# Kernel optimization log

Hardware: AMD Instinct MI355X
Metric: run time of the kernel (lower is better)

Reference implementation:

```python
import jax, jax.numpy as jnp
import numpy as np

# Module constants from __init__: z_max=32, ppm=2 -> delta=0.5, z_min=delta=0.5, log_prob=True
Z_MIN = 0.5
Z_MAX = 32.0
DELTA = 0.5


def _depth_positions(S):
    # depth_steps = arange(z_min, z_max + delta, delta) -> Z=64 bins in [0.5, 32]
    depth_steps = jnp.arange(Z_MIN, Z_MAX + DELTA, DELTA)
    log_steps = jnp.log2(depth_steps)
    log_min = np.log2(Z_MIN)
    log_max = np.log2(Z_MAX)
    norm = (log_steps - log_min) / (log_max - log_min)  # in [0, 1]
    # grid_sample align_corners=True maps [-1,1] -> [0, S-1]; norm*2-1 -> norm*(S-1)
    return norm * (S - 1)  # (Z,)


def setup_inputs() -> dict:
    key = jax.random.key(0)
    k1, k2 = jax.random.split(key)
    image = jax.random.normal(k1, (32, 64, 64, 128), dtype=jnp.float32)          # (B,D,H,W)
    polar_log_depths = jax.random.normal(k2, (32, 64, 128, 64), dtype=jnp.float32)  # (B,H,W,S)
    return {"image": image, "polar_log_depths": polar_log_depths}


def reference(image, polar_log_depths):
    S = polar_log_depths.shape[-1]
    pos = _depth_positions(S)                                 # (Z,) fixed interp positions
    i0 = jnp.clip(jnp.floor(pos).astype(jnp.int32), 0, S - 1)
    i1 = jnp.clip(i0 + 1, 0, S - 1)
    w = pos - i0.astype(pos.dtype)                            # linear weights; w=0 at right edge
    v0 = jnp.take(polar_log_depths, i0, axis=-1)              # (B,H,W,Z)
    v1 = jnp.take(polar_log_depths, i1, axis=-1)
    depth_scores = v0 * (1.0 - w) + v1 * w                    # 1D linear interp == grid_sample here

    # log_prob=True branch: softmax / logsumexp over height axis (dim=1)
    depth_prob = jax.nn.softmax(depth_scores, axis=1)         # (B,H,W,Z)
    cell_score = jax.nn.logsumexp(depth_scores, axis=1)       # (B,W,Z)

    # einsum '...dhw,...hwz->...dzw': weighted reduction over height
    image_polar = jnp.einsum('bdhw,bhwz->bdzw', image, depth_prob)  # (B,D,Z,W)
    return image_polar, cell_score
```

## Files before the change

### kernel.cpp

```cpp
#include <hip/hip_runtime.h>
#include <hip/hip_bf16.h>
#include <math.h>

#define B_ 32
#define D_ 64
#define H_ 64
#define W_ 128
#define S_ 64
#define Z_ 64
#define WT 4

typedef __attribute__((ext_vector_type(8))) short bf16x8;
typedef __attribute__((ext_vector_type(4))) float f32x4;

static __device__ __forceinline__ short f2bf(float f) {
    union { __hip_bfloat16 h; short s; } u;
    u.h = __float2bfloat16(f);
    return u.s;
}
static __device__ __forceinline__ float getc(const float4& v, int k) {
    switch (k) { case 0: return v.x; case 1: return v.y; case 2: return v.z; default: return v.w; }
}

static __device__ __forceinline__ int swz(int w, int row, int oct) {
    return w * 8192 + row * 128 + (((oct ^ row ^ w) & 7) << 4);
}

__global__ __launch_bounds__(1024, 8)
void polar_proj_kernel(const float* __restrict__ image,
                       const float* __restrict__ polar,
                       float* __restrict__ out_img,
                       float* __restrict__ out_cell) {
    __shared__ __align__(16) unsigned char sP[WT * 8192];
    __shared__ __align__(16) unsigned char sA[WT * 8192];

    const int t = threadIdx.x;

    const int cpx = gridDim.x >> 3;
    const int logical = (blockIdx.x & 7) * cpx + (blockIdx.x >> 3);
    const int b  = logical >> 5;
    const int w0 = (logical & 31) << 2;

    const int d_im = t >> 4;
    const int h0   = (t & 15) << 2;
    float4 ir[4];
#pragma unroll
    for (int k = 0; k < 4; ++k)
        ir[k] = *(const float4*)(image + ((size_t)((b * D_ + d_im) * H_ + h0 + k)) * W_ + w0);

    const int q4  = t & 3;
    const int rr  = t >> 2;
    const int w_p = rr >> 6, h_p = rr & 63;
    const float* src = polar + ((size_t)((b * H_ + h_p) * W_ + w0 + w_p)) * S_ + q4 * 16;
    float4 pr[4];
#pragma unroll
    for (int k = 0; k < 4; ++k)
        pr[k] = *(const float4*)(src + k * 4);

#pragma unroll
    for (int w = 0; w < 4; ++w) {
        const short s0 = f2bf(getc(ir[0], w));
        const short s1 = f2bf(getc(ir[1], w));
        const short s2 = f2bf(getc(ir[2], w));
        const short s3 = f2bf(getc(ir[3], w));
        int2 pk;
        pk.x = (s0 & 0xffff) | (s1 << 16);
        pk.y = (s2 & 0xffff) | (s3 << 16);
        *(int2*)(sA + swz(w, d_im, h0 >> 3) + ((h0 & 7) << 1)) = pk;
    }

#pragma unroll
    for (int c = 0; c < 2; ++c) {
        bf16x8 v;
#pragma unroll
        for (int e = 0; e < 8; ++e)
            v[e] = f2bf(getc(pr[c * 2 + (e >> 2)], e & 3));
        *(bf16x8*)(sP + swz(w_p, h_p, q4 * 2 + c)) = v;
    }
    __syncthreads();

    const int lane = t & 63;
    const int wv   = t >> 6;
    const int fr   = lane & 15, lg = lane >> 4;
    const int wS   = wv >> 2, zq = wv & 3;

    const int z = zq * 16 + fr;
    const float posf = (log2f(0.5f + 0.5f * (float)z) + 1.0f) * 10.5f;
    int i0 = (int)floorf(posf);
    i0 = i0 < 0 ? 0 : (i0 > S_ - 1 ? S_ - 1 : i0);
    const int i1 = (i0 + 1 > S_ - 1) ? (S_ - 1) : (i0 + 1);
    const float wz = posf - (float)i0;

    bf16x8 bw[2];
#pragma unroll
    for (int ks = 0; ks < 2; ++ks)
#pragma unroll
        for (int e = 0; e < 8; ++e) {
            const int s = ks * 32 + lg * 8 + e;
            const float v = (s == i0 ? 1.0f - wz : 0.0f) + (s == i1 ? wz : 0.0f);
            bw[ks][e] = f2bf(v);
        }

    f32x4 sacc[4] = {};
#pragma unroll
    for (int ks = 0; ks < 2; ++ks)
#pragma unroll
        for (int mt = 0; mt < 4; ++mt) {
            const bf16x8 a = *(const bf16x8*)(sP + swz(wS, mt * 16 + fr, ks * 4 + lg));
            sacc[mt] = __builtin_amdgcn_mfma_f32_16x16x32_bf16(a, bw[ks], sacc[mt], 0, 0, 0);
        }

    float ex[4][4];
    float ss = 0.0f;
#pragma unroll
    for (int mt = 0; mt < 4; ++mt)
#pragma unroll
        for (int r = 0; r < 4; ++r) {
            const float e = __expf(sacc[mt][r]);
            ex[mt][r] = e;
            ss += e;
        }
    ss += __shfl_xor(ss, 16);
    ss += __shfl_xor(ss, 32);
    if (lg == 0)
        out_cell[((size_t)b * W_ + w0 + wS) * Z_ + z] = __logf(ss);
    const float inv = 1.0f / ss;
    __syncthreads();

#pragma unroll
    for (int mt = 0; mt < 4; ++mt) {
        const short p0 = f2bf(ex[mt][0] * inv);
        const short p1 = f2bf(ex[mt][1] * inv);
        const short p2 = f2bf(ex[mt][2] * inv);
        const short p3 = f2bf(ex[mt][3] * inv);
        int2 pk;
        pk.x = (p0 & 0xffff) | (p1 << 16);
        pk.y = (p2 & 0xffff) | (p3 << 16);
        *(int2*)(sP + swz(wS, z, mt * 2 + (lg >> 1)) + ((lg & 1) << 3)) = pk;
    }
    __syncthreads();

    const int mtp = wv >> 2, ntp = wv & 3;
    f32x4 acc[4] = {};
#pragma unroll
    for (int w = 0; w < 4; ++w)
#pragma unroll
        for (int ks = 0; ks < 2; ++ks) {
            const bf16x8 a  = *(const bf16x8*)(sA + swz(w, mtp * 16 + fr, ks * 4 + lg));
            const bf16x8 bb = *(const bf16x8*)(sP + swz(w, ntp * 16 + fr, ks * 4 + lg));
            acc[w] = __builtin_amdgcn_mfma_f32_16x16x32_bf16(a, bb, acc[w], 0, 0, 0);
        }

#pragma unroll
    for (int r = 0; r < 4; ++r) {
        const int d  = mtp * 16 + lg * 4 + r;
        const int zc = ntp * 16 + fr;
        float4 o;
        o.x = acc[0][r];
        o.y = acc[1][r];
        o.z = acc[2][r];
        o.w = acc[3][r];
        *(float4*)(out_img + ((size_t)((b * D_ + d) * Z_) + zc) * W_ + w0) = o;
    }
}

extern "C" void kernel_launch(void* const* d_in, const int* in_sizes, int n_in,
                              void* d_out, int out_size, void* d_ws, size_t ws_size,
                              hipStream_t stream) {
    const float* image = (const float*)d_in[0];
    const float* polar = (const float*)d_in[1];
    float* out_img  = (float*)d_out;
    float* out_cell = out_img + (size_t)B_ * D_ * Z_ * W_;
    dim3 grid(B_ * (W_ / WT));
    polar_proj_kernel<<<grid, 1024, 0, stream>>>(image, polar, out_img, out_cell);
}
```

Measured before the change: 51.12 us.

## Split into softmax-prob kernel and wide-W PV matmul kernel with stashed probabilities

The single fused kernel becomes two. The first computes the interpolated scores, the softmax and the logsumexp, then writes bf16 probabilities into the output buffer as a scratch stash. The second loads a 16-wide W slab of the image, reads the stashed probabilities, runs the MFMA reduction over height, and transposes the results through LDS so each output row is written as a wider contiguous segment. The aim is to replace the scattered 16-byte output stores with wider coalesced ones, at the cost of an extra global write and read of the probabilities, a second launch, and lower occupancy from the larger LDS footprint.

After: 56.78 us. +11.1%, slower.

```diff
diff --git a/kernel.cpp b/kernel.cpp
--- a/kernel.cpp
+++ b/kernel.cpp
@@ -8,7 +8,6 @@
 #define W_ 128
 #define S_ 64
 #define Z_ 64
-#define WT 4
 
 typedef __attribute__((ext_vector_type(8))) short bf16x8;
 typedef __attribute__((ext_vector_type(4))) float f32x4;
@@ -27,48 +26,26 @@
 }
 
 __global__ __launch_bounds__(1024, 8)
-void polar_proj_kernel(const float* __restrict__ image,
-                       const float* __restrict__ polar,
+void polar_prob_kernel(const float* __restrict__ polar,
                        float* __restrict__ out_img,
                        float* __restrict__ out_cell) {
-    __shared__ __align__(16) unsigned char sP[WT * 8192];
-    __shared__ __align__(16) unsigned char sA[WT * 8192];
+    __shared__ __align__(16) unsigned char sP[4 * 8192];
 
     const int t = threadIdx.x;
-
     const int cpx = gridDim.x >> 3;
     const int logical = (blockIdx.x & 7) * cpx + (blockIdx.x >> 3);
-    const int b  = logical >> 5;
-    const int w0 = (logical & 31) << 2;
-
-    const int d_im = t >> 4;
-    const int h0   = (t & 15) << 2;
-    float4 ir[4];
-#pragma unroll
-    for (int k = 0; k < 4; ++k)
-        ir[k] = *(const float4*)(image + ((size_t)((b * D_ + d_im) * H_ + h0 + k)) * W_ + w0);
-
-    const int q4  = t & 3;
-    const int rr  = t >> 2;
+    const int b   = logical >> 5;
+    const int wt4 = logical & 31;
+    const int w0  = wt4 << 2;
+
+    const int q4 = t & 3;
+    const int rr = t >> 2;
     const int w_p = rr >> 6, h_p = rr & 63;
     const float* src = polar + ((size_t)((b * H_ + h_p) * W_ + w0 + w_p)) * S_ + q4 * 16;
     float4 pr[4];
 #pragma unroll
     for (int k = 0; k < 4; ++k)
         pr[k] = *(const float4*)(src + k * 4);
-
-#pragma unroll
-    for (int w = 0; w < 4; ++w) {
-        const short s0 = f2bf(getc(ir[0], w));
-        const short s1 = f2bf(getc(ir[1], w));
-        const short s2 = f2bf(getc(ir[2], w));
-        const short s3 = f2bf(getc(ir[3], w));
-        int2 pk;
-        pk.x = (s0 & 0xffff) | (s1 << 16);
-        pk.y = (s2 & 0xffff) | (s3 << 16);
-        *(int2*)(sA + swz(w, d_im, h0 >> 3) + ((h0 & 7) << 1)) = pk;
-    }
-
 #pragma unroll
     for (int c = 0; c < 2; ++c) {
         bf16x8 v;
@@ -83,8 +60,7 @@
     const int wv   = t >> 6;
     const int fr   = lane & 15, lg = lane >> 4;
     const int wS   = wv >> 2, zq = wv & 3;
-
-    const int z = zq * 16 + fr;
+    const int z    = zq * 16 + fr;
     const float posf = (log2f(0.5f + 0.5f * (float)z) + 1.0f) * 10.5f;
     int i0 = (int)floorf(posf);
     i0 = i0 < 0 ? 0 : (i0 > S_ - 1 ? S_ - 1 : i0);
@@ -140,27 +116,97 @@
     }
     __syncthreads();
 
-    const int mtp = wv >> 2, ntp = wv & 3;
-    f32x4 acc[4] = {};
-#pragma unroll
-    for (int w = 0; w < 4; ++w)
+    const int octid = wt4 >> 2;
+    const int wsub  = (wt4 & 3) << 2;
+    const int w0B   = octid << 4;
+#pragma unroll
+    for (int p = 0; p < 2; ++p) {
+        const int u  = t + p * 1024;
+        const int wl = u >> 9, zz = (u >> 3) & 63, oc = u & 7;
+        const float4 v = *(const float4*)(sP + swz(wl, zz, oc));
+        const int ws = wsub + wl;
+        float* dst = out_img
+            + ((size_t)((b * 64 + ws * 2 + (zz >> 5)) * 64 + ((zz & 31) * 2 + (oc >> 2)))) * 128
+            + w0B + ((oc & 3) << 2);
+        *(float4*)dst = v;
+    }
+}
+
+__global__ __launch_bounds__(1024, 4)
+void polar_pv_kernel(const float* __restrict__ image,
+                     const float* stash,
+                     float* out_img) {
+    __shared__ __align__(16) unsigned char sA[16 * 8192];
+
+    const int t = threadIdx.x;
+    const int cpx = gridDim.x >> 3;
+    const int logical = (blockIdx.x & 7) * cpx + (blockIdx.x >> 3);
+    const int b   = logical >> 3;
+    const int oct = logical & 7;
+    const int w0B = oct << 4;
+
+    const int wq = t & 3;
+#pragma unroll
+    for (int p = 0; p < 4; ++p) {
+        const int unit = p * 256 + (t >> 2);
+        const int d = unit >> 4, hq = unit & 15;
+        float4 v[4];
+#pragma unroll
+        for (int k = 0; k < 4; ++k)
+            v[k] = *(const float4*)(image + ((size_t)((b * D_ + d) * H_ + hq * 4 + k)) * W_ + w0B + wq * 4);
+#pragma unroll
+        for (int c = 0; c < 4; ++c) {
+            const int wl = wq * 4 + c;
+            int2 pk;
+            pk.x = (f2bf(getc(v[0], c)) & 0xffff) | (f2bf(getc(v[1], c)) << 16);
+            pk.y = (f2bf(getc(v[2], c)) & 0xffff) | (f2bf(getc(v[3], c)) << 16);
+            *(int2*)(sA + swz(wl, d, hq >> 1) + ((hq & 1) << 3)) = pk;
+        }
+    }
+    __syncthreads();
+
+    const int lane = t & 63;
+    const int wv   = t >> 6;
+    const int fr   = lane & 15, lg = lane >> 4;
+    const int dt   = wv >> 2, zt = wv & 3;
+    const int z    = zt * 16 + fr;
+    const int rowA = dt * 16 + fr;
+    const float* pbase = stash
+        + ((size_t)((b * 64 + (z >> 5)) * 64 + (z & 31) * 2)) * 128
+        + w0B + (lg << 2);
+
+    f32x4 acc[16] = {};
+#pragma unroll
+    for (int w = 0; w < 16; ++w)
 #pragma unroll
         for (int ks = 0; ks < 2; ++ks) {
-            const bf16x8 a  = *(const bf16x8*)(sA + swz(w, mtp * 16 + fr, ks * 4 + lg));
-            const bf16x8 bb = *(const bf16x8*)(sP + swz(w, ntp * 16 + fr, ks * 4 + lg));
+            const bf16x8 a  = *(const bf16x8*)(sA + swz(w, rowA, ks * 4 + lg));
+            const bf16x8 bb = *(const bf16x8*)(pbase + w * 16384 + ks * 128);
             acc[w] = __builtin_amdgcn_mfma_f32_16x16x32_bf16(a, bb, acc[w], 0, 0, 0);
         }
-
+    __syncthreads();
+
+    unsigned char* rg = sA + wv * 5120;
+    const int dzw = lg * 16 + fr;
 #pragma unroll
     for (int r = 0; r < 4; ++r) {
-        const int d  = mtp * 16 + lg * 4 + r;
-        const int zc = ntp * 16 + fr;
-        float4 o;
-        o.x = acc[0][r];
-        o.y = acc[1][r];
-        o.z = acc[2][r];
-        o.w = acc[3][r];
-        *(float4*)(out_img + ((size_t)((b * D_ + d) * Z_) + zc) * W_ + w0) = o;
+#pragma unroll
+        for (int j = 0; j < 4; ++j) {
+            float4 v;
+            v.x = acc[j * 4 + 0][r];
+            v.y = acc[j * 4 + 1][r];
+            v.z = acc[j * 4 + 2][r];
+            v.w = acc[j * 4 + 3][r];
+            *(float4*)(rg + dzw * 80 + j * 16) = v;
+        }
+#pragma unroll
+        for (int i = 0; i < 4; ++i) {
+            const int dzr = i * 16 + (lane >> 2);
+            const float4 o = *(const float4*)(rg + dzr * 80 + (lane & 3) * 16);
+            const int d  = dt * 16 + i * 4 + r;
+            const int zz = zt * 16 + (lane >> 2);
+            *(float4*)(out_img + ((size_t)((b * D_ + d) * Z_ + zz)) * W_ + w0B + (lane & 3) * 4) = o;
+        }
     }
 }
 
@@ -171,6 +217,7 @@
     const float* polar = (const float*)d_in[1];
     float* out_img  = (float*)d_out;
     float* out_cell = out_img + (size_t)B_ * D_ * Z_ * W_;
-    dim3 grid(B_ * (W_ / WT));
-    polar_proj_kernel<<<grid, 1024, 0, stream>>>(image, polar, out_img, out_cell);
-}
+    (void)d_ws; (void)ws_size;
+    polar_prob_kernel<<<dim3(1024), 1024, 0, stream>>>(polar, out_img, out_cell);
+    polar_pv_kernel<<<dim3(256), 1024, 0, stream>>>(image, out_img, out_img);
+}
```

## Process two W-tiles per block with prefetched loads for the second tile

Applied to the files above, without the earlier changes.

Each block now handles two consecutive 4-column W tiles, using double LDS buffers. The global loads for the second tile are issued before the first tile's compute, so their latency overlaps the first tile's MFMA work. Grid size is halved and LDS per block doubles to 128KB, which lowers the number of resident blocks (launch bounds drop to 4) and may reduce occupancy-based latency hiding. The per-tile computation is moved into helper functions without changing its logic.

Measured after the change: 59.10 us. 1.16x slower.

```diff
diff --git a/kernel.cpp b/kernel.cpp
--- a/kernel.cpp
+++ b/kernel.cpp
@@ -8,7 +8,6 @@
 #define W_ 128
 #define S_ 64
 #define Z_ 64
-#define WT 4
 
 typedef __attribute__((ext_vector_type(8))) short bf16x8;
 typedef __attribute__((ext_vector_type(4))) float f32x4;
@@ -26,64 +25,53 @@
     return w * 8192 + row * 128 + (((oct ^ row ^ w) & 7) << 4);
 }
 
-__global__ __launch_bounds__(1024, 8)
-void polar_proj_kernel(const float* __restrict__ image,
-                       const float* __restrict__ polar,
-                       float* __restrict__ out_img,
-                       float* __restrict__ out_cell) {
-    __shared__ __align__(16) unsigned char sP[WT * 8192];
-    __shared__ __align__(16) unsigned char sA[WT * 8192];
-
-    const int t = threadIdx.x;
-
-    const int cpx = gridDim.x >> 3;
-    const int logical = (blockIdx.x & 7) * cpx + (blockIdx.x >> 3);
-    const int b  = logical >> 5;
-    const int w0 = (logical & 31) << 2;
-
+struct Regs { float4 ir[4]; float4 pr[4]; };
+
+static __device__ __forceinline__ void issue_loads(const float* __restrict__ image,
+                                                   const float* __restrict__ polar,
+                                                   int b, int w0, int t, Regs& r) {
     const int d_im = t >> 4;
     const int h0   = (t & 15) << 2;
-    float4 ir[4];
 #pragma unroll
     for (int k = 0; k < 4; ++k)
-        ir[k] = *(const float4*)(image + ((size_t)((b * D_ + d_im) * H_ + h0 + k)) * W_ + w0);
-
-    const int q4  = t & 3;
-    const int rr  = t >> 2;
+        r.ir[k] = *(const float4*)(image + ((size_t)((b * D_ + d_im) * H_ + h0 + k)) * W_ + w0);
+    const int q4 = t & 3;
+    const int rr = t >> 2;
     const int w_p = rr >> 6, h_p = rr & 63;
     const float* src = polar + ((size_t)((b * H_ + h_p) * W_ + w0 + w_p)) * S_ + q4 * 16;
-    float4 pr[4];
 #pragma unroll
     for (int k = 0; k < 4; ++k)
-        pr[k] = *(const float4*)(src + k * 4);
-
+        r.pr[k] = *(const float4*)(src + k * 4);
+}
+
+static __device__ __forceinline__ void lds_write(unsigned char* sP, unsigned char* sA,
+                                                 int t, const Regs& r) {
+    const int d_im = t >> 4;
+    const int h0   = (t & 15) << 2;
 #pragma unroll
     for (int w = 0; w < 4; ++w) {
-        const short s0 = f2bf(getc(ir[0], w));
-        const short s1 = f2bf(getc(ir[1], w));
-        const short s2 = f2bf(getc(ir[2], w));
-        const short s3 = f2bf(getc(ir[3], w));
         int2 pk;
-        pk.x = (s0 & 0xffff) | (s1 << 16);
-        pk.y = (s2 & 0xffff) | (s3 << 16);
+        pk.x = (f2bf(getc(r.ir[0], w)) & 0xffff) | (f2bf(getc(r.ir[1], w)) << 16);
+        pk.y = (f2bf(getc(r.ir[2], w)) & 0xffff) | (f2bf(getc(r.ir[3], w)) << 16);
         *(int2*)(sA + swz(w, d_im, h0 >> 3) + ((h0 & 7) << 1)) = pk;
     }
-
+    const int q4 = t & 3;
+    const int rr = t >> 2;
+    const int w_p = rr >> 6, h_p = rr & 63;
 #pragma unroll
     for (int c = 0; c < 2; ++c) {
         bf16x8 v;
 #pragma unroll
         for (int e = 0; e < 8; ++e)
-            v[e] = f2bf(getc(pr[c * 2 + (e >> 2)], e & 3));
+            v[e] = f2bf(getc(r.pr[c * 2 + (e >> 2)], e & 3));
         *(bf16x8*)(sP + swz(w_p, h_p, q4 * 2 + c)) = v;
     }
-    __syncthreads();
-
-    const int lane = t & 63;
-    const int wv   = t >> 6;
-    const int fr   = lane & 15, lg = lane >> 4;
-    const int wS   = wv >> 2, zq = wv & 3;
-
+}
+
+static __device__ __forceinline__ void s_phase(const unsigned char* sP, int b, int w0,
+                                               int wS, int zq, int fr, int lg,
+                                               float* __restrict__ out_cell,
+                                               float ex[4][4], float& inv) {
     const int z = zq * 16 + fr;
     const float posf = (log2f(0.5f + 0.5f * (float)z) + 1.0f) * 10.5f;
     int i0 = (int)floorf(posf);
@@ -110,7 +98,6 @@
             sacc[mt] = __builtin_amdgcn_mfma_f32_16x16x32_bf16(a, bw[ks], sacc[mt], 0, 0, 0);
         }
 
-    float ex[4][4];
     float ss = 0.0f;
 #pragma unroll
     for (int mt = 0; mt < 4; ++mt)
@@ -124,23 +111,25 @@
     ss += __shfl_xor(ss, 32);
     if (lg == 0)
         out_cell[((size_t)b * W_ + w0 + wS) * Z_ + z] = __logf(ss);
-    const float inv = 1.0f / ss;
-    __syncthreads();
-
+    inv = 1.0f / ss;
+}
+
+static __device__ __forceinline__ void pt_write(unsigned char* sP, int wS, int zq,
+                                                int fr, int lg,
+                                                const float ex[4][4], float inv) {
+    const int z = zq * 16 + fr;
 #pragma unroll
     for (int mt = 0; mt < 4; ++mt) {
-        const short p0 = f2bf(ex[mt][0] * inv);
-        const short p1 = f2bf(ex[mt][1] * inv);
-        const short p2 = f2bf(ex[mt][2] * inv);
-        const short p3 = f2bf(ex[mt][3] * inv);
         int2 pk;
-        pk.x = (p0 & 0xffff) | (p1 << 16);
-        pk.y = (p2 & 0xffff) | (p3 << 16);
+        pk.x = (f2bf(ex[mt][0] * inv) & 0xffff) | (f2bf(ex[mt][1] * inv) << 16);
+        pk.y = (f2bf(ex[mt][2] * inv) & 0xffff) | (f2bf(ex[mt][3] * inv) << 16);
         *(int2*)(sP + swz(wS, z, mt * 2 + (lg >> 1)) + ((lg & 1) << 3)) = pk;
     }
-    __syncthreads();
-
-    const int mtp = wv >> 2, ntp = wv & 3;
+}
+
+static __device__ __forceinline__ void pv_store(const unsigned char* sP, const unsigned char* sA,
+                                                int b, int w0, int mtp, int ntp, int fr, int lg,
+                                                float* __restrict__ out_img) {
     f32x4 acc[4] = {};
 #pragma unroll
     for (int w = 0; w < 4; ++w)
@@ -150,7 +139,6 @@
             const bf16x8 bb = *(const bf16x8*)(sP + swz(w, ntp * 16 + fr, ks * 4 + lg));
             acc[w] = __builtin_amdgcn_mfma_f32_16x16x32_bf16(a, bb, acc[w], 0, 0, 0);
         }
-
 #pragma unroll
     for (int r = 0; r < 4; ++r) {
         const int d  = mtp * 16 + lg * 4 + r;
@@ -164,6 +152,52 @@
     }
 }
 
+__global__ __launch_bounds__(1024, 4)
+void polar_fused2_kernel(const float* __restrict__ image,
+                         const float* __restrict__ polar,
+                         float* __restrict__ out_img,
+                         float* __restrict__ out_cell) {
+    __shared__ __align__(16) unsigned char sP0[4 * 8192];
+    __shared__ __align__(16) unsigned char sA0[4 * 8192];
+    __shared__ __align__(16) unsigned char sP1[4 * 8192];
+    __shared__ __align__(16) unsigned char sA1[4 * 8192];
+
+    const int t = threadIdx.x;
+    const int cpx = gridDim.x >> 3;
+    const int logical = (blockIdx.x & 7) * cpx + (blockIdx.x >> 3);
+    const int tile0 = logical << 1;
+    const int b   = tile0 >> 5;
+    const int w0a = (tile0 & 31) << 2;
+    const int w0b = w0a + 4;
+
+    const int lane = t & 63, wv = t >> 6;
+    const int fr = lane & 15, lg = lane >> 4;
+    const int wS = wv >> 2, zq = wv & 3;
+
+    Regs r0, r1;
+    issue_loads(image, polar, b, w0a, t, r0);
+    lds_write(sP0, sA0, t, r0);
+    issue_loads(image, polar, b, w0b, t, r1);
+    __syncthreads();
+
+    float ex0[4][4], inv0;
+    s_phase(sP0, b, w0a, wS, zq, fr, lg, out_cell, ex0, inv0);
+    __syncthreads();
+    pt_write(sP0, wS, zq, fr, lg, ex0, inv0);
+    __syncthreads();
+
+    pv_store(sP0, sA0, b, w0a, wS, zq, fr, lg, out_img);
+    lds_write(sP1, sA1, t, r1);
+    __syncthreads();
+
+    float ex1[4][4], inv1;
+    s_phase(sP1, b, w0b, wS, zq, fr, lg, out_cell, ex1, inv1);
+    __syncthreads();
+    pt_write(sP1, wS, zq, fr, lg, ex1, inv1);
+    __syncthreads();
+    pv_store(sP1, sA1, b, w0b, wS, zq, fr, lg, out_img);
+}
+
 extern "C" void kernel_launch(void* const* d_in, const int* in_sizes, int n_in,
                               void* d_out, int out_size, void* d_ws, size_t ws_size,
                               hipStream_t stream) {
@@ -171,6 +205,7 @@
     const float* polar = (const float*)d_in[1];
     float* out_img  = (float*)d_out;
     float* out_cell = out_img + (size_t)B_ * D_ * Z_ * W_;
-    dim3 grid(B_ * (W_ / WT));
-    polar_proj_kernel<<<grid, 1024, 0, stream>>>(image, polar, out_img, out_cell);
-}
+    (void)d_ws; (void)ws_size;
+    dim3 grid(B_ * (W_ / 4) / 2);
+    polar_fused2_kernel<<<grid, 1024, 0, stream>>>(image, polar, out_img, out_cell);
+}
```

## Load polar scores directly into MFMA registers and halve block size to 512 threads

Applied to the files above, without the earlier changes.

The polar depth scores are now read from global memory straight into MFMA A-operand registers, skipping the LDS staging pass and one block-wide barrier. The block shrinks from 1024 to 512 threads, so each wave handles two z-tiles in both the interpolation and the einsum MFMAs, reusing each loaded A fragment twice. Image staging is split into two passes per thread. The trade-off is more registers per thread and global loads laid out in MFMA fragment order, which may coalesce less well than the old contiguous reads.

Result: slower. 56.54 us (+10.6%).

```diff
diff --git a/kernel.cpp b/kernel.cpp
--- a/kernel.cpp
+++ b/kernel.cpp
@@ -8,7 +8,6 @@
 #define W_ 128
 #define S_ 64
 #define Z_ 64
-#define WT 4
 
 typedef __attribute__((ext_vector_type(8))) short bf16x8;
 typedef __attribute__((ext_vector_type(4))) float f32x4;
@@ -21,147 +20,151 @@
 static __device__ __forceinline__ float getc(const float4& v, int k) {
     switch (k) { case 0: return v.x; case 1: return v.y; case 2: return v.z; default: return v.w; }
 }
+static __device__ __forceinline__ bf16x8 cvt8(const float4& a, const float4& b) {
+    bf16x8 v;
+    v[0] = f2bf(a.x); v[1] = f2bf(a.y); v[2] = f2bf(a.z); v[3] = f2bf(a.w);
+    v[4] = f2bf(b.x); v[5] = f2bf(b.y); v[6] = f2bf(b.z); v[7] = f2bf(b.w);
+    return v;
+}
 
 static __device__ __forceinline__ int swz(int w, int row, int oct) {
     return w * 8192 + row * 128 + (((oct ^ row ^ w) & 7) << 4);
 }
 
-__global__ __launch_bounds__(1024, 8)
-void polar_proj_kernel(const float* __restrict__ image,
-                       const float* __restrict__ polar,
-                       float* __restrict__ out_img,
-                       float* __restrict__ out_cell) {
-    __shared__ __align__(16) unsigned char sP[WT * 8192];
-    __shared__ __align__(16) unsigned char sA[WT * 8192];
+__global__ __launch_bounds__(512, 4)
+void polar_fused1b_kernel(const float* __restrict__ image,
+                          const float* __restrict__ polar,
+                          float* __restrict__ out_img,
+                          float* __restrict__ out_cell) {
+    __shared__ __align__(16) unsigned char sA[4 * 8192];
+    __shared__ __align__(16) unsigned char sP[4 * 8192];
 
     const int t = threadIdx.x;
-
     const int cpx = gridDim.x >> 3;
     const int logical = (blockIdx.x & 7) * cpx + (blockIdx.x >> 3);
     const int b  = logical >> 5;
     const int w0 = (logical & 31) << 2;
 
-    const int d_im = t >> 4;
-    const int h0   = (t & 15) << 2;
-    float4 ir[4];
-#pragma unroll
-    for (int k = 0; k < 4; ++k)
-        ir[k] = *(const float4*)(image + ((size_t)((b * D_ + d_im) * H_ + h0 + k)) * W_ + w0);
-
-    const int q4  = t & 3;
-    const int rr  = t >> 2;
-    const int w_p = rr >> 6, h_p = rr & 63;
-    const float* src = polar + ((size_t)((b * H_ + h_p) * W_ + w0 + w_p)) * S_ + q4 * 16;
-    float4 pr[4];
-#pragma unroll
-    for (int k = 0; k < 4; ++k)
-        pr[k] = *(const float4*)(src + k * 4);
+    const int lane = t & 63, wv = t >> 6;
+    const int fr = lane & 15, lg = lane >> 4;
 
 #pragma unroll
-    for (int w = 0; w < 4; ++w) {
-        const short s0 = f2bf(getc(ir[0], w));
-        const short s1 = f2bf(getc(ir[1], w));
-        const short s2 = f2bf(getc(ir[2], w));
-        const short s3 = f2bf(getc(ir[3], w));
-        int2 pk;
-        pk.x = (s0 & 0xffff) | (s1 << 16);
-        pk.y = (s2 & 0xffff) | (s3 << 16);
-        *(int2*)(sA + swz(w, d_im, h0 >> 3) + ((h0 & 7) << 1)) = pk;
+    for (int p = 0; p < 2; ++p) {
+        const int u  = p * 512 + t;
+        const int d  = u >> 4;
+        const int h0 = (u & 15) << 2;
+        float4 ir[4];
+#pragma unroll
+        for (int k = 0; k < 4; ++k)
+            ir[k] = *(const float4*)(image + ((size_t)((b * D_ + d) * H_ + h0 + k)) * W_ + w0);
+#pragma unroll
+        for (int w = 0; w < 4; ++w) {
+            int2 pk;
+            pk.x = (f2bf(getc(ir[0], w)) & 0xffff) | (f2bf(getc(ir[1], w)) << 16);
+            pk.y = (f2bf(getc(ir[2], w)) & 0xffff) | (f2bf(getc(ir[3], w)) << 16);
+            *(int2*)(sA + swz(w, d, h0 >> 3) + ((h0 & 7) << 1)) = pk;
+        }
+    }
+
+    const int wS = wv >> 1, zh = wv & 1;
+
+    bf16x8 bw[2][2];
+    float  invz[2];
+#pragma unroll
+    for (int zt = 0; zt < 2; ++zt) {
+        const int z = zh * 32 + zt * 16 + fr;
+        const float posf = (log2f(0.5f + 0.5f * (float)z) + 1.0f) * 10.5f;
+        int i0 = (int)floorf(posf);
+        i0 = i0 < 0 ? 0 : (i0 > S_ - 1 ? S_ - 1 : i0);
+        const int i1 = (i0 + 1 > S_ - 1) ? (S_ - 1) : (i0 + 1);
+        const float wz = posf - (float)i0;
+#pragma unroll
+        for (int ks = 0; ks < 2; ++ks)
+#pragma unroll
+            for (int e = 0; e < 8; ++e) {
+                const int s = ks * 32 + lg * 8 + e;
+                const float v = (s == i0 ? 1.0f - wz : 0.0f) + (s == i1 ? wz : 0.0f);
+                bw[ks][zt][e] = f2bf(v);
+            }
+    }
+
+    const float* pb = polar + ((size_t)((b * H_ + fr) * W_) + (w0 + wS)) * S_ + lg * 8;
+
+    f32x4 sacc[4][2] = {};
+#pragma unroll
+    for (int mt = 0; mt < 4; ++mt) {
+        const float* pm = pb + (size_t)mt * 16 * W_ * S_;
+        const float4 c00 = *(const float4*)(pm);
+        const float4 c01 = *(const float4*)(pm + 4);
+        const float4 c10 = *(const float4*)(pm + 32);
+        const float4 c11 = *(const float4*)(pm + 36);
+        const bf16x8 a0 = cvt8(c00, c01);
+        const bf16x8 a1 = cvt8(c10, c11);
+        sacc[mt][0] = __builtin_amdgcn_mfma_f32_16x16x32_bf16(a0, bw[0][0], sacc[mt][0], 0, 0, 0);
+        sacc[mt][0] = __builtin_amdgcn_mfma_f32_16x16x32_bf16(a1, bw[1][0], sacc[mt][0], 0, 0, 0);
+        sacc[mt][1] = __builtin_amdgcn_mfma_f32_16x16x32_bf16(a0, bw[0][1], sacc[mt][1], 0, 0, 0);
+        sacc[mt][1] = __builtin_amdgcn_mfma_f32_16x16x32_bf16(a1, bw[1][1], sacc[mt][1], 0, 0, 0);
     }
 
 #pragma unroll
-    for (int c = 0; c < 2; ++c) {
-        bf16x8 v;
+    for (int zt = 0; zt < 2; ++zt) {
+        float ss = 0.0f;
 #pragma unroll
-        for (int e = 0; e < 8; ++e)
-            v[e] = f2bf(getc(pr[c * 2 + (e >> 2)], e & 3));
-        *(bf16x8*)(sP + swz(w_p, h_p, q4 * 2 + c)) = v;
+        for (int mt = 0; mt < 4; ++mt)
+#pragma unroll
+            for (int r = 0; r < 4; ++r) {
+                const float e = __expf(sacc[mt][zt][r]);
+                sacc[mt][zt][r] = e;
+                ss += e;
+            }
+        ss += __shfl_xor(ss, 16);
+        ss += __shfl_xor(ss, 32);
+        if (lg == 0)
+            out_cell[((size_t)b * W_ + w0 + wS) * Z_ + zh * 32 + zt * 16 + fr] = __logf(ss);
+        invz[zt] = 1.0f / ss;
+    }
+
+#pragma unroll
+    for (int zt = 0; zt < 2; ++zt) {
+        const int zrow = zh * 32 + zt * 16 + fr;
+        const float inv = invz[zt];
+#pragma unroll
+        for (int mt = 0; mt < 4; ++mt) {
+            int2 pk;
+            pk.x = (f2bf(sacc[mt][zt][0] * inv) & 0xffff) | (f2bf(sacc[mt][zt][1] * inv) << 16);
+            pk.y = (f2bf(sacc[mt][zt][2] * inv) & 0xffff) | (f2bf(sacc[mt][zt][3] * inv) << 16);
+            *(int2*)(sP + swz(wS, zrow, mt * 2 + (lg >> 1)) + ((lg & 1) << 3)) = pk;
+        }
     }
     __syncthreads();
 
-    const int lane = t & 63;
-    const int wv   = t >> 6;
-    const int fr   = lane & 15, lg = lane >> 4;
-    const int wS   = wv >> 2, zq = wv & 3;
-
-    const int z = zq * 16 + fr;
-    const float posf = (log2f(0.5f + 0.5f * (float)z) + 1.0f) * 10.5f;
-    int i0 = (int)floorf(posf);
-    i0 = i0 < 0 ? 0 : (i0 > S_ - 1 ? S_ - 1 : i0);
-    const int i1 = (i0 + 1 > S_ - 1) ? (S_ - 1) : (i0 + 1);
-    const float wz = posf - (float)i0;
-
-    bf16x8 bw[2];
-#pragma unroll
-    for (int ks = 0; ks < 2; ++ks)
-#pragma unroll
-        for (int e = 0; e < 8; ++e) {
-            const int s = ks * 32 + lg * 8 + e;
-            const float v = (s == i0 ? 1.0f - wz : 0.0f) + (s == i1 ? wz : 0.0f);
-            bw[ks][e] = f2bf(v);
-        }
-
-    f32x4 sacc[4] = {};
-#pragma unroll
-    for (int ks = 0; ks < 2; ++ks)
-#pragma unroll
-        for (int mt = 0; mt < 4; ++mt) {
-            const bf16x8 a = *(const bf16x8*)(sP + swz(wS, mt * 16 + fr, ks * 4 + lg));
-            sacc[mt] = __builtin_amdgcn_mfma_f32_16x16x32_bf16(a, bw[ks], sacc[mt], 0, 0, 0);
-        }
-
-    float ex[4][4];
-    float ss = 0.0f;
-#pragma unroll
-    for (int mt = 0; mt < 4; ++mt)
-#pragma unroll
-        for (int r = 0; r < 4; ++r) {
-            const float e = __expf(sacc[mt][r]);
-            ex[mt][r] = e;
-            ss += e;
-        }
-    ss += __shfl_xor(ss, 16);
-    ss += __shfl_xor(ss, 32);
-    if (lg == 0)
-        out_cell[((size_t)b * W_ + w0 + wS) * Z_ + z] = __logf(ss);
-    const float inv = 1.0f / ss;
-    __syncthreads();
-
-#pragma unroll
-    for (int mt = 0; mt < 4; ++mt) {
-        const short p0 = f2bf(ex[mt][0] * inv);
-        const short p1 = f2bf(ex[mt][1] * inv);
-        const short p2 = f2bf(ex[mt][2] * inv);
-        const short p3 = f2bf(ex[mt][3] * inv);
-        int2 pk;
-        pk.x = (p0 & 0xffff) | (p1 << 16);
-        pk.y = (p2 & 0xffff) | (p3 << 16);
-        *(int2*)(sP + swz(wS, z, mt * 2 + (lg >> 1)) + ((lg & 1) << 3)) = pk;
-    }
-    __syncthreads();
-
-    const int mtp = wv >> 2, ntp = wv & 3;
-    f32x4 acc[4] = {};
+    const int mtp = wv >> 1, ntq = wv & 1;
+    f32x4 acc[4][2] = {};
 #pragma unroll
     for (int w = 0; w < 4; ++w)
 #pragma unroll
         for (int ks = 0; ks < 2; ++ks) {
-            const bf16x8 a  = *(const bf16x8*)(sA + swz(w, mtp * 16 + fr, ks * 4 + lg));
-            const bf16x8 bb = *(const bf16x8*)(sP + swz(w, ntp * 16 + fr, ks * 4 + lg));
-            acc[w] = __builtin_amdgcn_mfma_f32_16x16x32_bf16(a, bb, acc[w], 0, 0, 0);
+            const bf16x8 a = *(const bf16x8*)(sA + swz(w, mtp * 16 + fr, ks * 4 + lg));
+#pragma unroll
+            for (int zz = 0; zz < 2; ++zz) {
+                const bf16x8 bb = *(const bf16x8*)(sP + swz(w, ntq * 32 + zz * 16 + fr, ks * 4 + lg));
+                acc[w][zz] = __builtin_amdgcn_mfma_f32_16x16x32_bf16(a, bb, acc[w][zz], 0, 0, 0);
+            }
         }
 
 #pragma unroll
-    for (int r = 0; r < 4; ++r) {
-        const int d  = mtp * 16 + lg * 4 + r;
-        const int zc = ntp * 16 + fr;
-        float4 o;
-        o.x = acc[0][r];
-        o.y = acc[1][r];
-        o.z = acc[2][r];
-        o.w = acc[3][r];
-        *(float4*)(out_img + ((size_t)((b * D_ + d) * Z_) + zc) * W_ + w0) = o;
-    }
+    for (int zz = 0; zz < 2; ++zz)
+#pragma unroll
+        for (int r = 0; r < 4; ++r) {
+            const int d = mtp * 16 + lg * 4 + r;
+            const int z = ntq * 32 + zz * 16 + fr;
+            float4 o;
+            o.x = acc[0][zz][r];
+            o.y = acc[1][zz][r];
+            o.z = acc[2][zz][r];
+            o.w = acc[3][zz][r];
+            *(float4*)(out_img + ((size_t)((b * D_ + d) * Z_) + z) * W_ + w0) = o;
+        }
 }
 
 extern "C" void kernel_launch(void* const* d_in, const int* in_sizes, int n_in,
@@ -171,6 +174,7 @@
     const float* polar = (const float*)d_in[1];
     float* out_img  = (float*)d_out;
     float* out_cell = out_img + (size_t)B_ * D_ * Z_ * W_;
-    dim3 grid(B_ * (W_ / WT));
-    polar_proj_kernel<<<grid, 1024, 0, stream>>>(image, polar, out_img, out_cell);
+    (void)d_ws; (void)ws_size;
+    dim3 grid(B_ * (W_ / 4));
+    polar_fused1b_kernel<<<grid, 512, 0, stream>>>(image, polar, out_img, out_cell);
 }
```
